# Kernel optimization log

Measured on AMD Instinct MI355X. Metric: run time of the kernel, lower is better.

The kernel has to match this reference:

```python
import jax, jax.numpy as jnp
import numpy as np

T, B, V, H = 128, 64, 8192, 2048

def setup_inputs() -> dict:
    key = jax.random.key(0)
    k1, k2, k3, k4, k5 = jax.random.split(key, 5)
    inputs = jax.random.randint(k1, (T, B), 0, V, dtype=jnp.int64)
    hidden_w = jax.random.normal(k2, (H, V + H), dtype=jnp.float32) * 0.02
    hidden_b = jax.random.normal(k3, (H,), dtype=jnp.float32) * 0.02
    output_w = jax.random.normal(k4, (V, H), dtype=jnp.float32) * 0.02
    output_b = jax.random.normal(k5, (V,), dtype=jnp.float32) * 0.02
    return {"inputs": inputs, "hidden_w": hidden_w, "hidden_b": hidden_b,
            "output_w": output_w, "output_b": output_b}

def reference(inputs, hidden_w, hidden_b, output_w, output_b):
    vocab = output_w.shape[0]
    num_hiddens = hidden_w.shape[0]
    batch = inputs.shape[1]
    state0 = jnp.zeros((batch, num_hiddens), dtype=jnp.float32)

    def step(state, x):
        # x: (B,) int token ids -> one-hot (B, V)
        emb = jax.nn.one_hot(x, vocab, dtype=jnp.float32)
        combined = jnp.concatenate([emb, state], axis=1)       # (B, V+H)
        new_state = jnp.tanh(combined @ hidden_w.T + hidden_b)  # (B, H)
        out = new_state @ output_w.T + output_b                 # (B, V)
        return new_state, out

    final_state, outputs = jax.lax.scan(step, state0, inputs)
    # outputs: (T, B, V) — stacked version of the original's list of per-step outputs
    return outputs, final_state
```

## Files before the change

kernel.cpp:

```cpp
#include <hip/hip_runtime.h>

#define T_STEPS 128
#define BATCH   64
#define VOCAB   8192
#define HID     2048
#define WROW    (VOCAB + HID)
#define BH      (BATCH * HID)
#define CNT_STRIDE 512

typedef __bf16 bf16_t;
typedef __bf16 bf16x8 __attribute__((ext_vector_type(8)));
typedef float  f32x4  __attribute__((ext_vector_type(4)));
typedef unsigned long long u64;

__global__ void conv_whh(const float* __restrict__ hw, bf16_t* __restrict__ whh,
                         int* __restrict__ cnt) {
    if (blockIdx.x == 0) {
        for (int i = threadIdx.x; i < 4 * CNT_STRIDE; i += 256) cnt[i] = 0;
    }
    int idx = blockIdx.x * 256 + threadIdx.x;
    int i4 = idx * 4;
    int h = i4 >> 11;
    int j = i4 & 2047;
    float4 w = *(const float4*)(hw + (size_t)h * WROW + VOCAB + j);
    union { bf16_t b[4]; uint2 u; } t;
    t.b[0] = (bf16_t)w.x; t.b[1] = (bf16_t)w.y; t.b[2] = (bf16_t)w.z; t.b[3] = (bf16_t)w.w;
    *(uint2*)(whh + (size_t)h * HID + j) = t.u;
}

__global__ void conv_wout(const float* __restrict__ wo, bf16_t* __restrict__ wob) {
    size_t i4 = ((size_t)blockIdx.x * 256 + threadIdx.x) * 4;
    float4 w = *(const float4*)(wo + i4);
    union { bf16_t b[4]; uint2 u; } t;
    t.b[0] = (bf16_t)w.x; t.b[1] = (bf16_t)w.y; t.b[2] = (bf16_t)w.z; t.b[3] = (bf16_t)w.w;
    *(uint2*)(wob + i4) = t.u;
}

__global__ void trans_emb(const float* __restrict__ hw, bf16_t* __restrict__ wt) {
    __shared__ float tile[32][33];
    int tx = threadIdx.x, ty = threadIdx.y;
    int v0 = blockIdx.x * 32, h0 = blockIdx.y * 32;
#pragma unroll
    for (int i = 0; i < 4; i++)
        tile[ty + i * 8][tx] = hw[(size_t)(h0 + ty + i * 8) * WROW + v0 + tx];
    __syncthreads();
#pragma unroll
    for (int i = 0; i < 4; i++)
        wt[(size_t)(v0 + ty + i * 8) * HID + h0 + tx] = (bf16_t)tile[tx][ty + i * 8];
}

__launch_bounds__(512)
__global__ void rnn_persist(bf16_t* __restrict__ states,
                            const bf16_t* __restrict__ whh,
                            const bf16_t* __restrict__ wembT,
                            const float* __restrict__ hb,
                            const int* __restrict__ toks,
                            float* __restrict__ fin,
                            int* __restrict__ cnt) {
    __shared__ float part[8][512];

    const int tid = threadIdx.x;
    const int w = tid >> 6, lane = tid & 63;
    const int q = lane >> 4, l15 = lane & 15;
    const int bm = blockIdx.x & 3, bn = blockIdx.x >> 2;
    const int m0 = bm * 16, n0 = bn * 32;
    const int kb = w * 256;

    bf16x8 breg[2][8];
#pragma unroll
    for (int nt = 0; nt < 2; nt++)
#pragma unroll
        for (int kk = 0; kk < 8; kk++)
            breg[nt][kk] = *(const bf16x8*)(
                whh + (size_t)(n0 + nt * 16 + l15) * HID + kb + kk * 32 + q * 8);

    const size_t abase8 = (size_t)((m0 + l15) * HID + kb + q * 8) >> 2;

    const int er = tid >> 4, ec = (tid & 15) * 2;
    const int R = m0 + er, h = n0 + ec;
    float bias0 = 0.f, bias1 = 0.f;
    if (tid < 256) { bias0 = hb[h]; bias1 = hb[h + 1]; }
    int* grpCnt = cnt + bm * CNT_STRIDE;

    for (int t = 0; t < T_STEPS; ++t) {
        float emb0 = 0.f, emb1 = 0.f;
        if (tid < 256) {
            int tok = toks[t * BATCH + R];
            emb0 = (float)wembT[(size_t)tok * HID + h];
            emb1 = (float)wembT[(size_t)tok * HID + h + 1];
        }

        f32x4 acc0 = (f32x4){0.f, 0.f, 0.f, 0.f};
        f32x4 acc1 = (f32x4){0.f, 0.f, 0.f, 0.f};
        if (t > 0) {
            if (tid == 0) {
                while (__hip_atomic_load(&grpCnt[t], __ATOMIC_RELAXED,
                                         __HIP_MEMORY_SCOPE_SYSTEM) < 64)
                    __builtin_amdgcn_s_sleep(1);
            }
            __syncthreads();
            asm volatile("" ::: "memory");

            const u64* sprev = (const u64*)(states + (size_t)t * BH);
            u64 a8[16];
#pragma unroll
            for (int kk = 0; kk < 8; kk++) {
                a8[2 * kk]     = __hip_atomic_load(sprev + abase8 + kk * 8,
                                    __ATOMIC_RELAXED, __HIP_MEMORY_SCOPE_SYSTEM);
                a8[2 * kk + 1] = __hip_atomic_load(sprev + abase8 + kk * 8 + 1,
                                    __ATOMIC_RELAXED, __HIP_MEMORY_SCOPE_SYSTEM);
            }
#pragma unroll
            for (int kk = 0; kk < 8; kk++) {
                union { u64 u[2]; bf16x8 v; } cv;
                cv.u[0] = a8[2 * kk]; cv.u[1] = a8[2 * kk + 1];
                acc0 = __builtin_amdgcn_mfma_f32_16x16x32_bf16(cv.v, breg[0][kk], acc0, 0, 0, 0);
                acc1 = __builtin_amdgcn_mfma_f32_16x16x32_bf16(cv.v, breg[1][kk], acc1, 0, 0, 0);
            }
        }
#pragma unroll
        for (int i = 0; i < 4; i++) {
            part[w][(q * 4 + i) * 32 + l15]      = acc0[i];
            part[w][(q * 4 + i) * 32 + 16 + l15] = acc1[i];
        }
        __syncthreads();
        if (tid < 256) {
            float s0 = 0.f, s1 = 0.f;
#pragma unroll
            for (int ww = 0; ww < 8; ww++) {
                float2 p = *(const float2*)&part[ww][er * 32 + ec];
                s0 += p.x; s1 += p.y;
            }
            float v0 = tanhf(s0 + emb0 + bias0);
            float v1 = tanhf(s1 + emb1 + bias1);
            union { bf16_t b[2]; unsigned int u; } pk;
            pk.b[0] = (bf16_t)v0; pk.b[1] = (bf16_t)v1;
            __hip_atomic_store(
                (unsigned int*)(states + (size_t)(t + 1) * BH + R * HID + h),
                pk.u, __ATOMIC_RELAXED, __HIP_MEMORY_SCOPE_SYSTEM);
            if (t == T_STEPS - 1)
                *(float2*)&fin[R * HID + h] = make_float2(v0, v1);
        }
        __syncthreads();
        asm volatile("" ::: "memory");
        if (tid == 0)
            __hip_atomic_fetch_add(&grpCnt[t + 1], 1, __ATOMIC_RELAXED,
                                   __HIP_MEMORY_SCOPE_SYSTEM);
    }
}

__launch_bounds__(256)
__global__ void out_gemm(const bf16_t* __restrict__ A,
                         const bf16_t* __restrict__ Bw,
                         const float* __restrict__ bias,
                         float* __restrict__ out) {
    __shared__ uint4 AsU[2][128 * 5];
    __shared__ uint4 BsU[2][128 * 5];
    const int tid = threadIdx.x;
    const int wv = tid >> 6, lane = tid & 63;
    const int wm = wv >> 1, wn = wv & 1;
    const int q = lane >> 4, l15 = lane & 15;
    const int bm = blockIdx.y, bn = blockIdx.x;

    const uint4* gA = (const uint4*)A + (size_t)bm * 128 * 256;
    const uint4* gB = (const uint4*)Bw + (size_t)bn * 128 * 256;

    f32x4 acc[4][4];
#pragma unroll
    for (int mt = 0; mt < 4; mt++)
#pragma unroll
        for (int nt = 0; nt < 4; nt++)
            acc[mt][nt] = (f32x4){0.f, 0.f, 0.f, 0.f};

    uint4 pa[2], pb[2];
#pragma unroll
    for (int i = 0; i < 2; i++) {
        int v = tid + 256 * i;
        pa[i] = gA[(v >> 2) * 256 + (v & 3)];
        pb[i] = gB[(v >> 2) * 256 + (v & 3)];
    }
#pragma unroll
    for (int i = 0; i < 2; i++) {
        int v = tid + 256 * i;
        AsU[0][(v >> 2) * 5 + (v & 3)] = pa[i];
        BsU[0][(v >> 2) * 5 + (v & 3)] = pb[i];
    }
    __syncthreads();

    for (int it = 0; it < 64; ++it) {
        int cur = it & 1;
        if (it < 63) {
            int k0v = (it + 1) * 4;
#pragma unroll
            for (int i = 0; i < 2; i++) {
                int v = tid + 256 * i;
                pa[i] = gA[(v >> 2) * 256 + k0v + (v & 3)];
                pb[i] = gB[(v >> 2) * 256 + k0v + (v & 3)];
            }
        }
        bf16x8 af[4], bfr[4];
#pragma unroll
        for (int mt = 0; mt < 4; mt++)
            af[mt] = *(const bf16x8*)&AsU[cur][(wm * 64 + mt * 16 + l15) * 5 + q];
#pragma unroll
        for (int nt = 0; nt < 4; nt++)
            bfr[nt] = *(const bf16x8*)&BsU[cur][(wn * 64 + nt * 16 + l15) * 5 + q];
#pragma unroll
        for (int mt = 0; mt < 4; mt++)
#pragma unroll
            for (int nt = 0; nt < 4; nt++)
                acc[mt][nt] = __builtin_amdgcn_mfma_f32_16x16x32_bf16(
                    af[mt], bfr[nt], acc[mt][nt], 0, 0, 0);
        if (it < 63) {
            int nxt = cur ^ 1;
#pragma unroll
            for (int i = 0; i < 2; i++) {
                int v = tid + 256 * i;
                AsU[nxt][(v >> 2) * 5 + (v & 3)] = pa[i];
                BsU[nxt][(v >> 2) * 5 + (v & 3)] = pb[i];
            }
        }
        __syncthreads();
    }

#pragma unroll
    for (int nt = 0; nt < 4; nt++) {
        int col = bn * 128 + wn * 64 + nt * 16 + l15;
        float bv = bias[col];
#pragma unroll
        for (int mt = 0; mt < 4; mt++) {
#pragma unroll
            for (int i = 0; i < 4; i++) {
                int row = bm * 128 + wm * 64 + mt * 16 + q * 4 + i;
                out[(size_t)row * 8192 + col] = acc[mt][nt][i] + bv;
            }
        }
    }
}

extern "C" void kernel_launch(void* const* d_in, const int* in_sizes, int n_in,
                              void* d_out, int out_size, void* d_ws, size_t ws_size,
                              hipStream_t stream) {
    const int*   toks = (const int*)d_in[0];
    const float* hw   = (const float*)d_in[1];
    const float* hb   = (const float*)d_in[2];
    const float* wo   = (const float*)d_in[3];
    const float* ob   = (const float*)d_in[4];
    float* out = (float*)d_out;

    char* ws = (char*)d_ws;
    bf16_t* states = (bf16_t*)ws;
    bf16_t* whh    = (bf16_t*)(ws + 33816576ULL);
    bf16_t* woutb  = (bf16_t*)(ws + 33816576ULL + 8388608ULL);
    bf16_t* wembT  = (bf16_t*)(ws + 33816576ULL + 8388608ULL + 33554432ULL);
    int*    cnt    = (int*)ws;

    conv_whh<<<(HID * HID / 4) / 256, 256, 0, stream>>>(hw, whh, cnt);
    conv_wout<<<(VOCAB * HID / 4) / 256, 256, 0, stream>>>(wo, woutb);
    trans_emb<<<dim3(VOCAB / 32, HID / 32), dim3(32, 8), 0, stream>>>(hw, wembT);

    float* fin = out + (size_t)T_STEPS * BATCH * VOCAB;
    void* args[] = { (void*)&states, (void*)&whh, (void*)&wembT,
                     (void*)&hb, (void*)&toks, (void*)&fin, (void*)&cnt };
    hipLaunchCooperativeKernel((void*)rnn_persist, dim3(256), dim3(512),
                               args, 0, stream);

    out_gemm<<<dim3(64, 64), 256, 0, stream>>>(
        states + (size_t)BH, woutb, ob, out);
}
```

Before: 1.382 ms.

## Replace counter barrier with per-block flags and use direct global-to-LDS loads

The recurrent kernel now signals progress through per-block step flags. Wave 0 polls all 64 flags at once with a wave-wide vote, replacing the single atomic counter that 64 blocks incremented and one thread polled with sleeps. The embedding read is merged into one 32-bit load. The output GEMM stages tiles with global_load_lds straight into unpadded LDS, skipping the register round-trip, but the unpadded layout may cause LDS bank conflicts on fragment reads. Correctness also relies on the async LDS loads being complete at the existing __syncthreads.

```diff
diff --git a/kernel.cpp b/kernel.cpp
--- a/kernel.cpp
+++ b/kernel.cpp
@@ -12,6 +12,8 @@
 typedef __bf16 bf16x8 __attribute__((ext_vector_type(8)));
 typedef float  f32x4  __attribute__((ext_vector_type(4)));
 typedef unsigned long long u64;
+typedef const __attribute__((address_space(1))) unsigned int gu32;
+typedef __attribute__((address_space(3))) unsigned int lu32;
 
 __global__ void conv_whh(const float* __restrict__ hw, bf16_t* __restrict__ whh,
                          int* __restrict__ cnt) {
@@ -80,23 +82,26 @@
     const int R = m0 + er, h = n0 + ec;
     float bias0 = 0.f, bias1 = 0.f;
     if (tid < 256) { bias0 = hb[h]; bias1 = hb[h + 1]; }
-    int* grpCnt = cnt + bm * CNT_STRIDE;
+    int* flags = cnt + bm * 64;
 
     for (int t = 0; t < T_STEPS; ++t) {
         float emb0 = 0.f, emb1 = 0.f;
         if (tid < 256) {
             int tok = toks[t * BATCH + R];
-            emb0 = (float)wembT[(size_t)tok * HID + h];
-            emb1 = (float)wembT[(size_t)tok * HID + h + 1];
+            union { unsigned int u; bf16_t b[2]; } e;
+            e.u = *(const unsigned int*)(wembT + (size_t)tok * HID + h);
+            emb0 = (float)e.b[0]; emb1 = (float)e.b[1];
         }
 
         f32x4 acc0 = (f32x4){0.f, 0.f, 0.f, 0.f};
         f32x4 acc1 = (f32x4){0.f, 0.f, 0.f, 0.f};
         if (t > 0) {
-            if (tid == 0) {
-                while (__hip_atomic_load(&grpCnt[t], __ATOMIC_RELAXED,
-                                         __HIP_MEMORY_SCOPE_SYSTEM) < 64)
-                    __builtin_amdgcn_s_sleep(1);
+            if (w == 0) {
+                int v;
+                do {
+                    v = __hip_atomic_load(&flags[lane], __ATOMIC_RELAXED,
+                                          __HIP_MEMORY_SCOPE_SYSTEM);
+                } while (!__all(v >= t));
             }
             __syncthreads();
             asm volatile("" ::: "memory");
@@ -144,8 +149,8 @@
         __syncthreads();
         asm volatile("" ::: "memory");
         if (tid == 0)
-            __hip_atomic_fetch_add(&grpCnt[t + 1], 1, __ATOMIC_RELAXED,
-                                   __HIP_MEMORY_SCOPE_SYSTEM);
+            __hip_atomic_store(&flags[bn], t + 1, __ATOMIC_RELAXED,
+                               __HIP_MEMORY_SCOPE_SYSTEM);
     }
 }
 
@@ -154,16 +159,30 @@
                          const bf16_t* __restrict__ Bw,
                          const float* __restrict__ bias,
                          float* __restrict__ out) {
-    __shared__ uint4 AsU[2][128 * 5];
-    __shared__ uint4 BsU[2][128 * 5];
+    __shared__ bf16_t As[2][128 * 32];
+    __shared__ bf16_t Bs[2][128 * 32];
     const int tid = threadIdx.x;
     const int wv = tid >> 6, lane = tid & 63;
     const int wm = wv >> 1, wn = wv & 1;
     const int q = lane >> 4, l15 = lane & 15;
     const int bm = blockIdx.y, bn = blockIdx.x;
 
-    const uint4* gA = (const uint4*)A + (size_t)bm * 128 * 256;
-    const uint4* gB = (const uint4*)Bw + (size_t)bn * 128 * 256;
+    const bf16_t* gA = A  + (size_t)bm * 128 * 2048;
+    const bf16_t* gB = Bw + (size_t)bn * 128 * 2048;
+
+    const int sRow = lane >> 2;
+    const int sCol = (lane & 3) * 8;
+
+#define STAGE_TILE(dstBuf, gsrc, k0)                                          \
+    do {                                                                      \
+        _Pragma("unroll")                                                     \
+        for (int i_ = 0; i_ < 2; i_++) {                                      \
+            int chunk_ = i_ * 4 + wv;                                         \
+            __builtin_amdgcn_global_load_lds(                                 \
+                (gu32*)(gsrc + ((size_t)(chunk_ * 16 + sRow)) * 2048 + (k0) + sCol), \
+                (lu32*)(dstBuf + chunk_ * 16 * 32), 16, 0, 0);                \
+        }                                                                     \
+    } while (0)
 
     f32x4 acc[4][4];
 #pragma unroll
@@ -172,56 +191,33 @@
         for (int nt = 0; nt < 4; nt++)
             acc[mt][nt] = (f32x4){0.f, 0.f, 0.f, 0.f};
 
-    uint4 pa[2], pb[2];
-#pragma unroll
-    for (int i = 0; i < 2; i++) {
-        int v = tid + 256 * i;
-        pa[i] = gA[(v >> 2) * 256 + (v & 3)];
-        pb[i] = gB[(v >> 2) * 256 + (v & 3)];
-    }
-#pragma unroll
-    for (int i = 0; i < 2; i++) {
-        int v = tid + 256 * i;
-        AsU[0][(v >> 2) * 5 + (v & 3)] = pa[i];
-        BsU[0][(v >> 2) * 5 + (v & 3)] = pb[i];
-    }
+    STAGE_TILE(As[0], gA, 0);
+    STAGE_TILE(Bs[0], gB, 0);
     __syncthreads();
 
     for (int it = 0; it < 64; ++it) {
         int cur = it & 1;
         if (it < 63) {
-            int k0v = (it + 1) * 4;
-#pragma unroll
-            for (int i = 0; i < 2; i++) {
-                int v = tid + 256 * i;
-                pa[i] = gA[(v >> 2) * 256 + k0v + (v & 3)];
-                pb[i] = gB[(v >> 2) * 256 + k0v + (v & 3)];
-            }
+            int k0 = (it + 1) * 32;
+            STAGE_TILE(As[cur ^ 1], gA, k0);
+            STAGE_TILE(Bs[cur ^ 1], gB, k0);
         }
         bf16x8 af[4], bfr[4];
 #pragma unroll
         for (int mt = 0; mt < 4; mt++)
-            af[mt] = *(const bf16x8*)&AsU[cur][(wm * 64 + mt * 16 + l15) * 5 + q];
+            af[mt] = *(const bf16x8*)&As[cur][(wm * 64 + mt * 16 + l15) * 32 + q * 8];
 #pragma unroll
         for (int nt = 0; nt < 4; nt++)
-            bfr[nt] = *(const bf16x8*)&BsU[cur][(wn * 64 + nt * 16 + l15) * 5 + q];
+            bfr[nt] = *(const bf16x8*)&Bs[cur][(wn * 64 + nt * 16 + l15) * 32 + q * 8];
 #pragma unroll
         for (int mt = 0; mt < 4; mt++)
 #pragma unroll
             for (int nt = 0; nt < 4; nt++)
                 acc[mt][nt] = __builtin_amdgcn_mfma_f32_16x16x32_bf16(
                     af[mt], bfr[nt], acc[mt][nt], 0, 0, 0);
-        if (it < 63) {
-            int nxt = cur ^ 1;
-#pragma unroll
-            for (int i = 0; i < 2; i++) {
-                int v = tid + 256 * i;
-                AsU[nxt][(v >> 2) * 5 + (v & 3)] = pa[i];
-                BsU[nxt][(v >> 2) * 5 + (v & 3)] = pb[i];
-            }
-        }
         __syncthreads();
     }
+#undef STAGE_TILE
 
 #pragma unroll
     for (int nt = 0; nt < 4; nt++) {
```

Result: no change. 1.359 ms (-1.7%).
